# Kernel tuning notes

Hardware: AMD Instinct MI355X
Metric: run time of the kernel (lower is better)

The kernel has to match this reference:

```python
import math
import jax, jax.numpy as jnp
import numpy as np

HIDDEN = 1024
NUM_HEADS = 16
HEAD_DIM = HIDDEN // NUM_HEADS
B, S = 4, 2048


def setup_inputs() -> dict:
    key = jax.random.key(0)
    ks = jax.random.split(key, 10)
    sc_in = 1.0 / math.sqrt(HIDDEN)
    inp = {
        "query": jax.random.normal(ks[0], (B, S, HIDDEN), jnp.float32),
        "key": jax.random.normal(ks[1], (B, S, HIDDEN), jnp.float32),
        "value": jax.random.normal(ks[2], (B, S, HIDDEN), jnp.float32),
        "mask": jax.random.randint(ks[3], (B, S), 0, 2).astype(bool),
        # NOTE: ModuleList([Linear]*num_heads) shares ONE Linear across all heads.
        "Wq": jax.random.normal(ks[4], (HIDDEN, HEAD_DIM), jnp.float32) * sc_in,
        "bq": jnp.zeros((HEAD_DIM,), jnp.float32),
        "Wk": jax.random.normal(ks[5], (HIDDEN, HEAD_DIM), jnp.float32) * sc_in,
        "bk": jnp.zeros((HEAD_DIM,), jnp.float32),
        "Wv": jax.random.normal(ks[6], (HIDDEN, HEAD_DIM), jnp.float32) * sc_in,
        "bv": jnp.zeros((HEAD_DIM,), jnp.float32),
        "Wout": jax.random.normal(ks[7], (HIDDEN, HIDDEN), jnp.float32) * sc_in,
        "bout": jnp.zeros((HIDDEN,), jnp.float32),
        "seq_mask": 0,
    }
    return inp


def _layer_norm_scores(x, eps=1e-8):
    # torch.std is unbiased (ddof=1); is_train=False => no affine
    mean = jnp.mean(x, axis=-1, keepdims=True)
    sigma = jnp.std(x, axis=-1, keepdims=True, ddof=1)
    return (x - mean) / (sigma + eps)


def reference(query, key, value, mask, Wq, bq, Wk, bk, Wv, bv, Wout, bout, seq_mask):
    # All heads share identical weights -> compute one head, tile the concat.
    q = query @ Wq + bq          # [B,S,hd]
    k = key @ Wk + bk            # [B,S,hd]
    v = value @ Wv + bv          # [B,S,hd]
    scores = jnp.einsum("bqd,bkd->bqk", q, k) / math.sqrt(HIDDEN)  # [B,S,S]
    scores = _layer_norm_scores(scores)
    m = jnp.broadcast_to(mask[:, None, :], scores.shape)  # [B,S,S]
    if seq_mask:
        tri = jnp.triu(jnp.ones(scores.shape[-2:], bool), k=1)
        m = m | tri[None]
    # original fills with -1e-32 (effectively a no-op bug) -- reproduce exactly
    scores = scores + jnp.where(m, jnp.float32(-1e-32), jnp.float32(0.0))
    attn = jax.nn.softmax(scores, axis=-1)
    head = jnp.einsum("bqk,bkd->bqd", attn, v)   # [B,S,hd]
    attention = jnp.tile(head, (1, 1, NUM_HEADS))  # concat of identical heads
    return attention @ Wout + bout
```

## Files before the change

### kernel.cpp

```cpp
#include <hip/hip_runtime.h>
#include <math.h>

#define B_  4
#define S_  2048
#define H_  1024
#define D_  64
#define ROWS (B_*S_)
#define KSPLIT 16
#define LOG2E 1.4426950408889634f

typedef __attribute__((ext_vector_type(4))) float  floatx4;
typedef __attribute__((ext_vector_type(8))) short  short8;
typedef __attribute__((ext_vector_type(8))) __bf16 bf16x8;

#define WS_KSUM 0
#define WS_M    (WS_KSUM + B_*D_)
#define WS_A2   (WS_M + B_*D_*D_)
#define WS_C2   (WS_A2 + ROWS)
#define WS_SWP  (WS_C2 + ROWS)
#define WS_FEND (WS_SWP + KSPLIT*ROWS)
#define WB_QB  0
#define WB_KF  (WB_QB + ROWS*D_)
#define WB_VF  (WB_KF + ROWS*D_)
#define WB_WT  (WB_VF + ROWS*D_)
#define WB_WFF (WB_WT + 3*D_*H_)
#define WB_OP  (WB_WFF + H_*D_)
#define NZ2    (B_*D_ + B_*D_*D_)

__device__ __forceinline__ unsigned short f2bf(float f) {
    union { float f; unsigned u; } v; v.f = f;
    unsigned r = v.u + 0x7FFFu + ((v.u >> 16) & 1u);
    return (unsigned short)(r >> 16);
}
__device__ __forceinline__ short bfc(float f) {
    __bf16 h = (__bf16)f;
    short s; __builtin_memcpy(&s, &h, 2); return s;
}
__device__ __forceinline__ float bf2f(short s) {
    union { unsigned u; float f; } v;
    v.u = ((unsigned)(unsigned short)s) << 16; return v.f;
}
__device__ __forceinline__ bf16x8 ldb(const short* p) {
    union { short8 s; bf16x8 b; } u; u.s = *(const short8*)p; return u.b;
}
#define MFMA(a,b,c) __builtin_amdgcn_mfma_f32_16x16x32_bf16(a, b, c, 0, 0, 0)
__device__ __forceinline__ void lds_fence() {
    __builtin_amdgcn_wave_barrier();
    __builtin_amdgcn_s_waitcnt(0xc07f);
    __builtin_amdgcn_wave_barrier();
}

__global__ __launch_bounds__(256) void prep(
    const float* __restrict__ Wq, const float* __restrict__ Wk,
    const float* __restrict__ Wv, const float* __restrict__ Wout,
    float* __restrict__ wsf)
{
    __shared__ float tile[64][65];
    short* wsb = (short*)(wsf + WS_FEND);
    const int bx = blockIdx.x, t = threadIdx.x;
    if (bx < 96) {
        int idx = bx * 256 + t;
        int mat = idx >> 13, rem = idx & 8191;
        int kc = rem >> 8, nt = (rem >> 6) & 3, lane = rem & 63;
        int g = lane >> 4, l15 = lane & 15;
        const float* W = (mat == 0) ? Wq : (mat == 1) ? Wk : Wv;
        short8 fr;
        #pragma unroll
        for (int j = 0; j < 8; ++j)
            fr[j] = (short)f2bf(W[(size_t)(kc*32 + g*8 + j) * D_ + nt*16 + l15]);
        *(short8*)&wsb[WB_WT + (size_t)idx * 8] = fr;
    } else if (bx < 112) {
        int n0 = (bx - 96) * 64;
        int nn = t & 63, dg = t >> 6;
        for (int dd = 0; dd < 16; ++dd) {
            int d = dg * 16 + dd;
            float s = 0.0f;
            #pragma unroll
            for (int h = 0; h < 16; ++h)
                s += Wout[(size_t)(h * 64 + d) * H_ + n0 + nn];
            tile[d][nn] = s;
        }
        __syncthreads();
        #pragma unroll
        for (int u = 0; u < 2; ++u) {
            int s = 2*t + u;
            int ctl = s >> 7, h = (s >> 6) & 1, lane = s & 63;
            int g = lane >> 4, l2 = lane & 15;
            short8 fr;
            #pragma unroll
            for (int j = 0; j < 8; ++j)
                fr[j] = (short)f2bf(tile[h*32 + g*8 + j][ctl*16 + l2]);
            *(short8*)&wsb[WB_WFF + (size_t)((((n0 >> 4) + ctl)*2 + h)*64 + lane) * 8] = fr;
        }
    } else {
        int i = (bx - 112) * 256 + t;
        if (i < NZ2) wsf[WS_KSUM + i] = 0.0f;
    }
}

__global__ __launch_bounds__(256) void qkv_mfma(
    const float* __restrict__ query, const float* __restrict__ key,
    const float* __restrict__ value,
    const float* __restrict__ bq, const float* __restrict__ bk,
    const float* __restrict__ bvp, float* __restrict__ wsf)
{
    short* wsb = (short*)(wsf + WS_FEND);
    const int mat = blockIdx.y;
    const float* X    = (mat == 0) ? query : (mat == 1) ? key : value;
    const float* bias = (mat == 0) ? bq    : (mat == 1) ? bk  : bvp;
    const short* WT3 = wsb + WB_WT + (size_t)mat * (D_ * H_);

    const int t = threadIdx.x, w = t >> 6, lane = t & 63;
    const int l15 = lane & 15, g = lane >> 4;
    const int r0 = blockIdx.x * 32;
    const int mrow0 = (w >> 1) * 16;
    const int nt0 = (w & 1) * 2;

    __shared__ short xs[32][136];
    floatx4 acc[2] = {};

    for (int step = 0; step < 8; ++step) {
        __syncthreads();
        #pragma unroll
        for (int u = 0; u < 4; ++u) {
            int row = u * 8 + (t >> 5), col = (t & 31) * 4;
            float4 xv = *(const float4*)&X[(size_t)(r0 + row) * H_ + step * 128 + col];
            short4 pk;
            pk.x = bfc(xv.x); pk.y = bfc(xv.y); pk.z = bfc(xv.z); pk.w = bfc(xv.w);
            *(short4*)&xs[row][col] = pk;
        }
        __syncthreads();
        #pragma unroll
        for (int kk = 0; kk < 4; ++kk) {
            bf16x8 a = ldb(&xs[mrow0 + l15][kk * 32 + g * 8]);
            int kc = step * 4 + kk;
            #pragma unroll
            for (int n = 0; n < 2; ++n) {
                bf16x8 bf = ldb(&WT3[(size_t)((kc * 4) + nt0 + n) * 512 + lane * 8]);
                acc[n] = MFMA(a, bf, acc[n]);
            }
        }
    }

    if (mat == 0) {
        short* QB = wsb + WB_QB;
        #pragma unroll
        for (int n = 0; n < 2; ++n) {
            int col = (nt0 + n) * 16 + l15;
            float bb = bias[col];
            #pragma unroll
            for (int r = 0; r < 4; ++r)
                QB[(size_t)(r0 + mrow0 + 4*g + r) * D_ + col] = (short)f2bf(acc[n][r] + bb);
        }
    } else if (mat == 1) {
        short* KF = wsb + WB_KF;
        #pragma unroll
        for (int n = 0; n < 2; ++n) {
            int d = (nt0 + n) * 16 + l15;
            int kh = d >> 5, gk = (d >> 3) & 3, j = d & 7;
            float bb = bias[d];
            #pragma unroll
            for (int r = 0; r < 4; ++r) {
                int R = r0 + mrow0 + 4*g + r;
                KF[(size_t)(((R >> 4) * 2 + kh) * 64 + gk * 16 + (R & 15)) * 8 + j] =
                    (short)f2bf(acc[n][r] + bb);
            }
        }
    } else {
        short* VF = wsb + WB_VF;
        int R0 = r0 + mrow0 + 4*g;
        int kh = (R0 >> 5) & 1, gv = (R0 >> 3) & 3, j0 = R0 & 7, blk = R0 >> 6;
        #pragma unroll
        for (int n = 0; n < 2; ++n) {
            int d = (nt0 + n) * 16 + l15;
            int ntv = d >> 4;
            float bb = bias[d];
            short4 pk;
            pk.x = (short)f2bf(acc[n][0] + bb); pk.y = (short)f2bf(acc[n][1] + bb);
            pk.z = (short)f2bf(acc[n][2] + bb); pk.w = (short)f2bf(acc[n][3] + bb);
            *(short4*)&VF[(size_t)(((blk * 4 + ntv) * 2 + kh) * 64 + gv * 16 + (d & 15)) * 8 + j0] = pk;
        }
    }
}

__global__ __launch_bounds__(256) void kstats(float* __restrict__ wsf) {
    const short* KF = (short*)(wsf + WS_FEND) + WB_KF;
    const int b     = blockIdx.x >> 5;
    const int chunk = blockIdx.x & 31;
    const int keyblk0 = b * 128 + chunk * 4;

    __shared__ float kt[64][64];
    const int t = threadIdx.x;
    #pragma unroll
    for (int u = 0; u < 2; ++u) {
        int s = 2*t + u;
        int kb4 = s >> 7, kh = (s >> 6) & 1, lane2 = s & 63;
        int g2 = lane2 >> 4, l2 = lane2 & 15;
        short8 v = *(const short8*)&KF[(size_t)(((keyblk0 + kb4) * 2 + kh) * 64 + lane2) * 8];
        #pragma unroll
        for (int j = 0; j < 8; ++j)
            kt[kb4 * 16 + l2][kh * 32 + g2 * 8 + j] = bf2f(v[j]);
    }
    __syncthreads();

    const int td = t >> 4, te = t & 15;
    float acc[4][4] = {};
    for (int j = 0; j < 64; ++j) {
        float4 a  = *(const float4*)&kt[j][td*4];
        float4 bb = *(const float4*)&kt[j][te*4];
        float av[4] = {a.x, a.y, a.z, a.w};
        float bw[4] = {bb.x, bb.y, bb.z, bb.w};
        #pragma unroll
        for (int i = 0; i < 4; ++i)
            #pragma unroll
            for (int l = 0; l < 4; ++l)
                acc[i][l] += av[i] * bw[l];
    }
    float* M = wsf + WS_M + (size_t)b * D_ * D_;
    #pragma unroll
    for (int i = 0; i < 4; ++i)
        #pragma unroll
        for (int l = 0; l < 4; ++l)
            atomicAdd(&M[(td*4 + i) * D_ + te*4 + l], acc[i][l]);

    if (t < 64) {
        float s = 0.0f;
        for (int j = 0; j < 64; ++j) s += kt[j][t];
        atomicAdd(&wsf[WS_KSUM + b * D_ + t], s);
    }
}

__global__ __launch_bounds__(256) void rowstats(float* __restrict__ wsf) {
    const short* Qb = (short*)(wsf + WS_FEND) + WB_QB;
    const int t = threadIdx.x, w = t >> 6, lane = t & 63;
    const int q0 = blockIdx.x * 32 + w * 8;
    const int b  = q0 >> 11;
    const float* M = wsf + WS_M + (size_t)b * D_ * D_;

    float qv[8], y[8] = {};
    #pragma unroll
    for (int r = 0; r < 8; ++r) qv[r] = bf2f(Qb[(size_t)(q0 + r) * D_ + lane]);
    for (int d2 = 0; d2 < 64; ++d2) {
        float m = M[d2 * D_ + lane];
        #pragma unroll
        for (int r = 0; r < 8; ++r) y[r] += __shfl(qv[r], d2, 64) * m;
    }
    float kl = wsf[WS_KSUM + b * D_ + lane];
    float z[8], sv[8];
    #pragma unroll
    for (int r = 0; r < 8; ++r) { z[r] = y[r] * qv[r]; sv[r] = qv[r] * kl; }
    #pragma unroll
    for (int m = 1; m < 64; m <<= 1) {
        #pragma unroll
        for (int r = 0; r < 8; ++r) {
            z[r]  += __shfl_xor(z[r],  m, 64);
            sv[r] += __shfl_xor(sv[r], m, 64);
        }
    }
    #pragma unroll
    for (int r = 0; r < 8; ++r) {
        if (lane == r) {
            float sum   = sv[r] * (1.0f / 32.0f);
            float sumsq = z[r]  * (1.0f / 1024.0f);
            float mu  = sum * (1.0f / 2048.0f);
            float var = (sumsq - sum * sum * (1.0f / 2048.0f)) * (1.0f / 2047.0f);
            var = fmaxf(var, 0.0f);
            float inv = 1.0f / (sqrtf(var) + 1e-8f);
            wsf[WS_A2 + q0 + r] = inv * (LOG2E / 32.0f);
            wsf[WS_C2 + q0 + r] = -mu * inv * LOG2E;
        }
    }
}

__global__ __launch_bounds__(128, 3) void attention(float* __restrict__ wsf) {
    short* wsb = (short*)(wsf + WS_FEND);
    const short* Qb = wsb + WB_QB;
    const short* KF = wsb + WB_KF;
    const short* VF = wsb + WB_VF;
    __shared__ short P[2][32][72];

    const int t = threadIdx.x, w = t >> 6, lane = t & 63;
    const int l15 = lane & 15, g = lane >> 4;
    const int q0 = blockIdx.x * 64 + w * 32;
    const int b  = blockIdx.x >> 5;
    const int kb = blockIdx.y * (S_ / KSPLIT);

    bf16x8 bqf[2][2];
    float a2v[2], c2v[2];
    #pragma unroll
    for (int nt = 0; nt < 2; ++nt) {
        int q = q0 + nt*16 + l15;
        #pragma unroll
        for (int h = 0; h < 2; ++h)
            bqf[nt][h] = ldb(&Qb[(size_t)q * D_ + h*32 + g*8]);
        a2v[nt] = wsf[WS_A2 + q];
        c2v[nt] = wsf[WS_C2 + q];
    }

    floatx4 O[2][4] = {};
    float sacc[2] = {0.0f, 0.0f};
    short* Pw = &P[w][0][0];

    for (int kc = 0; kc < S_ / KSPLIT; kc += 64) {
        const int key0 = kb + kc;
        const int kblk16 = (b * S_ + key0) >> 4;
        const int kblk64 = (b * S_ + key0) >> 6;
        floatx4 Sc[4][2] = {};
        __builtin_amdgcn_s_setprio(1);
        #pragma unroll
        for (int kt = 0; kt < 4; ++kt) {
            bf16x8 ak0 = ldb(&KF[(size_t)(((kblk16 + kt) * 2 + 0) * 64 + lane) * 8]);
            bf16x8 ak1 = ldb(&KF[(size_t)(((kblk16 + kt) * 2 + 1) * 64 + lane) * 8]);
            #pragma unroll
            for (int nt = 0; nt < 2; ++nt) {
                Sc[kt][nt] = MFMA(ak0, bqf[nt][0], Sc[kt][nt]);
                Sc[kt][nt] = MFMA(ak1, bqf[nt][1], Sc[kt][nt]);
            }
        }
        __builtin_amdgcn_s_setprio(0);
        lds_fence();
        #pragma unroll
        for (int nt = 0; nt < 2; ++nt) {
            const float aa = a2v[nt], cc = c2v[nt];
            #pragma unroll
            for (int kt = 0; kt < 4; ++kt) {
                float w0 = __builtin_amdgcn_exp2f(fmaf(Sc[kt][nt][0], aa, cc));
                float w1 = __builtin_amdgcn_exp2f(fmaf(Sc[kt][nt][1], aa, cc));
                float w2 = __builtin_amdgcn_exp2f(fmaf(Sc[kt][nt][2], aa, cc));
                float w3 = __builtin_amdgcn_exp2f(fmaf(Sc[kt][nt][3], aa, cc));
                sacc[nt] += (w0 + w1) + (w2 + w3);
                short4 pk;
                pk.x = bfc(w0); pk.y = bfc(w1); pk.z = bfc(w2); pk.w = bfc(w3);
                *(short4*)&Pw[(nt*16 + l15) * 72 + kt*16 + 4*g] = pk;
            }
        }
        lds_fence();
        bf16x8 ap[2][2];
        #pragma unroll
        for (int mt = 0; mt < 2; ++mt)
            #pragma unroll
            for (int kh = 0; kh < 2; ++kh)
                ap[mt][kh] = ldb(&Pw[(mt*16 + l15) * 72 + kh*32 + g*8]);
        __builtin_amdgcn_s_setprio(1);
        #pragma unroll
        for (int nt = 0; nt < 4; ++nt) {
            #pragma unroll
            for (int kh = 0; kh < 2; ++kh) {
                bf16x8 bv = ldb(&VF[(size_t)(((kblk64 * 4 + nt) * 2 + kh) * 64 + lane) * 8]);
                #pragma unroll
                for (int mt = 0; mt < 2; ++mt)
                    O[mt][nt] = MFMA(ap[mt][kh], bv, O[mt][nt]);
            }
        }
        __builtin_amdgcn_s_setprio(0);
    }

    #pragma unroll
    for (int nt = 0; nt < 2; ++nt) {
        sacc[nt] += __shfl_xor(sacc[nt], 16, 64);
        sacc[nt] += __shfl_xor(sacc[nt], 32, 64);
    }
    if (lane < 16) {
        wsf[WS_SWP + blockIdx.y * ROWS + q0 + lane]      = sacc[0];
        wsf[WS_SWP + blockIdx.y * ROWS + q0 + 16 + lane] = sacc[1];
    }
    short* OP = wsb + WB_OP + ((size_t)blockIdx.y * ROWS + q0) * D_;
    #pragma unroll
    for (int mt = 0; mt < 2; ++mt)
        #pragma unroll
        for (int nt = 0; nt < 4; ++nt)
            #pragma unroll
            for (int r = 0; r < 4; ++r)
                OP[(size_t)(mt*16 + 4*g + r) * D_ + nt*16 + l15] =
                    (short)f2bf(O[mt][nt][r]);
}

__global__ __launch_bounds__(256) void outmm(
    const float* __restrict__ bout, const float* __restrict__ wsf,
    float* __restrict__ out)
{
    const short* wsb = (const short*)(wsf + WS_FEND);
    const short* OP  = wsb + WB_OP;
    const short* WFF = wsb + WB_WFF;
    __shared__ short hnF[2 * 64 * 8];

    const int t = threadIdx.x;
    const int row0 = blockIdx.x * 16;

    {
        const int r = t >> 4;
        const int c = (t & 15) * 4;
        const int row = row0 + r;
        float sw = 0.0f;
        #pragma unroll
        for (int p = 0; p < KSPLIT; ++p) sw += wsf[WS_SWP + p * ROWS + row];
        float inv = 1.0f / sw;
        float a0 = 0.f, a1 = 0.f, a2 = 0.f, a3 = 0.f;
        #pragma unroll
        for (int p = 0; p < KSPLIT; ++p) {
            short4 o = *(const short4*)&OP[((size_t)p * ROWS + row) * D_ + c];
            a0 += bf2f(o.x); a1 += bf2f(o.y); a2 += bf2f(o.z); a3 += bf2f(o.w);
        }
        short4 hn;
        hn.x = (short)f2bf(a0 * inv); hn.y = (short)f2bf(a1 * inv);
        hn.z = (short)f2bf(a2 * inv); hn.w = (short)f2bf(a3 * inv);
        int kh = c >> 5, gH = (c >> 3) & 3, j0 = c & 7;
        *(short4*)&hnF[(size_t)(kh * 64 + gH * 16 + r) * 8 + j0] = hn;
    }
    __syncthreads();

    const int w = t >> 6, lane = t & 63, l15 = lane & 15, g = lane >> 4;
    bf16x8 ah0 = ldb(&hnF[(size_t)(0 * 64 + lane) * 8]);
    bf16x8 ah1 = ldb(&hnF[(size_t)(1 * 64 + lane) * 8]);
    #pragma unroll
    for (int i = 0; i < 16; ++i) {
        int n16 = w * 16 + i;
        floatx4 acc = {};
        acc = MFMA(ah0, ldb(&WFF[(size_t)(n16 * 2 + 0) * 512 + lane * 8]), acc);
        acc = MFMA(ah1, ldb(&WFF[(size_t)(n16 * 2 + 1) * 512 + lane * 8]), acc);
        int col = n16 * 16 + l15;
        float bb = bout[col];
        #pragma unroll
        for (int r = 0; r < 4; ++r)
            out[(size_t)(row0 + 4*g + r) * H_ + col] = acc[r] + bb;
    }
}

extern "C" void kernel_launch(void* const* d_in, const int* in_sizes, int n_in,
                              void* d_out, int out_size, void* d_ws, size_t ws_size,
                              hipStream_t stream) {
    const float* query = (const float*)d_in[0];
    const float* key   = (const float*)d_in[1];
    const float* value = (const float*)d_in[2];
    const float* Wq   = (const float*)d_in[4];
    const float* bq   = (const float*)d_in[5];
    const float* Wk   = (const float*)d_in[6];
    const float* bk   = (const float*)d_in[7];
    const float* Wv   = (const float*)d_in[8];
    const float* bv   = (const float*)d_in[9];
    const float* Wout = (const float*)d_in[10];
    const float* bout = (const float*)d_in[11];

    float* ws  = (float*)d_ws;
    float* out = (float*)d_out;

    prep<<<177, 256, 0, stream>>>(Wq, Wk, Wv, Wout, ws);
    qkv_mfma<<<dim3(ROWS/32, 3), 256, 0, stream>>>(query, key, value, bq, bk, bv, ws);
    kstats<<<B_ * 32, 256, 0, stream>>>(ws);
    rowstats<<<ROWS/32, 256, 0, stream>>>(ws);
    attention<<<dim3(ROWS/64, KSPLIT), 128, 0, stream>>>(ws);
    outmm<<<ROWS/16, 256, 0, stream>>>(bout, ws, out);
}
```

Before: 204.0 us.

## Fuse split-K attention with output projection in one workgroup per query tile

Replaces the 16-way split-K attention kernel and the separate output-projection kernel with one kernel. Each 512-thread workgroup handles 16 query rows. Its 8 waves each cover 256 keys, and their partial O and row sums are reduced in LDS before the final Wout MFMA and store. This removes the global round trip of the bf16 partials and row sums, plus one launch. In exchange, each wave now reuses K/V across only 16 queries instead of 32, which raises K/V load traffic per MFMA, and the workgroup needs more LDS.

```diff
diff --git a/kernel.cpp b/kernel.cpp
--- a/kernel.cpp
+++ b/kernel.cpp
@@ -6,7 +6,6 @@
 #define H_  1024
 #define D_  64
 #define ROWS (B_*S_)
-#define KSPLIT 16
 #define LOG2E 1.4426950408889634f
 
 typedef __attribute__((ext_vector_type(4))) float  floatx4;
@@ -17,14 +16,12 @@
 #define WS_M    (WS_KSUM + B_*D_)
 #define WS_A2   (WS_M + B_*D_*D_)
 #define WS_C2   (WS_A2 + ROWS)
-#define WS_SWP  (WS_C2 + ROWS)
-#define WS_FEND (WS_SWP + KSPLIT*ROWS)
+#define WS_FEND (WS_C2 + ROWS)
 #define WB_QB  0
 #define WB_KF  (WB_QB + ROWS*D_)
 #define WB_VF  (WB_KF + ROWS*D_)
 #define WB_WT  (WB_VF + ROWS*D_)
 #define WB_WFF (WB_WT + 3*D_*H_)
-#define WB_OP  (WB_WFF + H_*D_)
 #define NZ2    (B_*D_ + B_*D_*D_)
 
 __device__ __forceinline__ unsigned short f2bf(float f) {
@@ -272,149 +269,109 @@
     }
 }
 
-__global__ __launch_bounds__(128, 3) void attention(float* __restrict__ wsf) {
+__global__ __launch_bounds__(512, 4) void attn_fused(
+    const float* __restrict__ bout, float* __restrict__ wsf,
+    float* __restrict__ out)
+{
     short* wsb = (short*)(wsf + WS_FEND);
-    const short* Qb = wsb + WB_QB;
-    const short* KF = wsb + WB_KF;
-    const short* VF = wsb + WB_VF;
-    __shared__ short P[2][32][72];
+    const short* Qb  = wsb + WB_QB;
+    const short* KF  = wsb + WB_KF;
+    const short* VF  = wsb + WB_VF;
+    const short* WFF = wsb + WB_WFF;
+
+    __shared__ short P[8][16][72];
+    __shared__ short OL[8][16][64];
+    __shared__ float sumwL[8][16];
+    __shared__ short hnF[2 * 64 * 8];
 
     const int t = threadIdx.x, w = t >> 6, lane = t & 63;
     const int l15 = lane & 15, g = lane >> 4;
-    const int q0 = blockIdx.x * 64 + w * 32;
-    const int b  = blockIdx.x >> 5;
-    const int kb = blockIdx.y * (S_ / KSPLIT);
-
-    bf16x8 bqf[2][2];
-    float a2v[2], c2v[2];
-    #pragma unroll
-    for (int nt = 0; nt < 2; ++nt) {
-        int q = q0 + nt*16 + l15;
-        #pragma unroll
-        for (int h = 0; h < 2; ++h)
-            bqf[nt][h] = ldb(&Qb[(size_t)q * D_ + h*32 + g*8]);
-        a2v[nt] = wsf[WS_A2 + q];
-        c2v[nt] = wsf[WS_C2 + q];
-    }
-
-    floatx4 O[2][4] = {};
-    float sacc[2] = {0.0f, 0.0f};
+    const int q0 = blockIdx.x * 16;
+    const int b  = blockIdx.x >> 7;
+
+    bf16x8 bqf0 = ldb(&Qb[(size_t)(q0 + l15) * D_ + 0*32 + g*8]);
+    bf16x8 bqf1 = ldb(&Qb[(size_t)(q0 + l15) * D_ + 1*32 + g*8]);
+    const float a2v = wsf[WS_A2 + q0 + l15];
+    const float c2v = wsf[WS_C2 + q0 + l15];
+
+    floatx4 O[4] = {};
+    float sacc = 0.0f;
     short* Pw = &P[w][0][0];
 
-    for (int kc = 0; kc < S_ / KSPLIT; kc += 64) {
-        const int key0 = kb + kc;
+    for (int kc = 0; kc < 256; kc += 64) {
+        const int key0 = w * 256 + kc;
         const int kblk16 = (b * S_ + key0) >> 4;
         const int kblk64 = (b * S_ + key0) >> 6;
-        floatx4 Sc[4][2] = {};
+        floatx4 Sc[4] = {};
         __builtin_amdgcn_s_setprio(1);
         #pragma unroll
         for (int kt = 0; kt < 4; ++kt) {
             bf16x8 ak0 = ldb(&KF[(size_t)(((kblk16 + kt) * 2 + 0) * 64 + lane) * 8]);
             bf16x8 ak1 = ldb(&KF[(size_t)(((kblk16 + kt) * 2 + 1) * 64 + lane) * 8]);
-            #pragma unroll
-            for (int nt = 0; nt < 2; ++nt) {
-                Sc[kt][nt] = MFMA(ak0, bqf[nt][0], Sc[kt][nt]);
-                Sc[kt][nt] = MFMA(ak1, bqf[nt][1], Sc[kt][nt]);
-            }
+            Sc[kt] = MFMA(ak0, bqf0, Sc[kt]);
+            Sc[kt] = MFMA(ak1, bqf1, Sc[kt]);
         }
         __builtin_amdgcn_s_setprio(0);
         lds_fence();
         #pragma unroll
-        for (int nt = 0; nt < 2; ++nt) {
-            const float aa = a2v[nt], cc = c2v[nt];
-            #pragma unroll
-            for (int kt = 0; kt < 4; ++kt) {
-                float w0 = __builtin_amdgcn_exp2f(fmaf(Sc[kt][nt][0], aa, cc));
-                float w1 = __builtin_amdgcn_exp2f(fmaf(Sc[kt][nt][1], aa, cc));
-                float w2 = __builtin_amdgcn_exp2f(fmaf(Sc[kt][nt][2], aa, cc));
-                float w3 = __builtin_amdgcn_exp2f(fmaf(Sc[kt][nt][3], aa, cc));
-                sacc[nt] += (w0 + w1) + (w2 + w3);
-                short4 pk;
-                pk.x = bfc(w0); pk.y = bfc(w1); pk.z = bfc(w2); pk.w = bfc(w3);
-                *(short4*)&Pw[(nt*16 + l15) * 72 + kt*16 + 4*g] = pk;
-            }
+        for (int kt = 0; kt < 4; ++kt) {
+            float w0 = __builtin_amdgcn_exp2f(fmaf(Sc[kt][0], a2v, c2v));
+            float w1 = __builtin_amdgcn_exp2f(fmaf(Sc[kt][1], a2v, c2v));
+            float w2 = __builtin_amdgcn_exp2f(fmaf(Sc[kt][2], a2v, c2v));
+            float w3 = __builtin_amdgcn_exp2f(fmaf(Sc[kt][3], a2v, c2v));
+            sacc += (w0 + w1) + (w2 + w3);
+            short4 pk;
+            pk.x = bfc(w0); pk.y = bfc(w1); pk.z = bfc(w2); pk.w = bfc(w3);
+            *(short4*)&Pw[l15 * 72 + kt*16 + 4*g] = pk;
         }
         lds_fence();
-        bf16x8 ap[2][2];
-        #pragma unroll
-        for (int mt = 0; mt < 2; ++mt)
-            #pragma unroll
-            for (int kh = 0; kh < 2; ++kh)
-                ap[mt][kh] = ldb(&Pw[(mt*16 + l15) * 72 + kh*32 + g*8]);
+        bf16x8 ap0 = ldb(&Pw[l15 * 72 + 0*32 + g*8]);
+        bf16x8 ap1 = ldb(&Pw[l15 * 72 + 1*32 + g*8]);
         __builtin_amdgcn_s_setprio(1);
         #pragma unroll
         for (int nt = 0; nt < 4; ++nt) {
-            #pragma unroll
-            for (int kh = 0; kh < 2; ++kh) {
-                bf16x8 bv = ldb(&VF[(size_t)(((kblk64 * 4 + nt) * 2 + kh) * 64 + lane) * 8]);
-                #pragma unroll
-                for (int mt = 0; mt < 2; ++mt)
-                    O[mt][nt] = MFMA(ap[mt][kh], bv, O[mt][nt]);
-            }
+            bf16x8 bv0 = ldb(&VF[(size_t)(((kblk64 * 4 + nt) * 2 + 0) * 64 + lane) * 8]);
+            bf16x8 bv1 = ldb(&VF[(size_t)(((kblk64 * 4 + nt) * 2 + 1) * 64 + lane) * 8]);
+            O[nt] = MFMA(ap0, bv0, O[nt]);
+            O[nt] = MFMA(ap1, bv1, O[nt]);
         }
         __builtin_amdgcn_s_setprio(0);
     }
 
-    #pragma unroll
-    for (int nt = 0; nt < 2; ++nt) {
-        sacc[nt] += __shfl_xor(sacc[nt], 16, 64);
-        sacc[nt] += __shfl_xor(sacc[nt], 32, 64);
-    }
-    if (lane < 16) {
-        wsf[WS_SWP + blockIdx.y * ROWS + q0 + lane]      = sacc[0];
-        wsf[WS_SWP + blockIdx.y * ROWS + q0 + 16 + lane] = sacc[1];
-    }
-    short* OP = wsb + WB_OP + ((size_t)blockIdx.y * ROWS + q0) * D_;
-    #pragma unroll
-    for (int mt = 0; mt < 2; ++mt)
-        #pragma unroll
-        for (int nt = 0; nt < 4; ++nt)
-            #pragma unroll
-            for (int r = 0; r < 4; ++r)
-                OP[(size_t)(mt*16 + 4*g + r) * D_ + nt*16 + l15] =
-                    (short)f2bf(O[mt][nt][r]);
-}
-
-__global__ __launch_bounds__(256) void outmm(
-    const float* __restrict__ bout, const float* __restrict__ wsf,
-    float* __restrict__ out)
-{
-    const short* wsb = (const short*)(wsf + WS_FEND);
-    const short* OP  = wsb + WB_OP;
-    const short* WFF = wsb + WB_WFF;
-    __shared__ short hnF[2 * 64 * 8];
-
-    const int t = threadIdx.x;
-    const int row0 = blockIdx.x * 16;
+    sacc += __shfl_xor(sacc, 16, 64);
+    sacc += __shfl_xor(sacc, 32, 64);
+    if (lane < 16) sumwL[w][lane] = sacc;
+    #pragma unroll
+    for (int nt = 0; nt < 4; ++nt)
+        #pragma unroll
+        for (int r = 0; r < 4; ++r)
+            OL[w][4*g + r][nt*16 + l15] = (short)f2bf(O[nt][r]);
+    __syncthreads();
 
     {
-        const int r = t >> 4;
-        const int c = (t & 15) * 4;
-        const int row = row0 + r;
-        float sw = 0.0f;
-        #pragma unroll
-        for (int p = 0; p < KSPLIT; ++p) sw += wsf[WS_SWP + p * ROWS + row];
+        const int row = t >> 5;
+        const int c = (t & 31) * 2;
+        float s0 = 0.f, s1 = 0.f, sw = 0.f;
+        #pragma unroll
+        for (int p = 0; p < 8; ++p) {
+            s0 += bf2f(OL[p][row][c]);
+            s1 += bf2f(OL[p][row][c + 1]);
+            sw += sumwL[p][row];
+        }
         float inv = 1.0f / sw;
-        float a0 = 0.f, a1 = 0.f, a2 = 0.f, a3 = 0.f;
-        #pragma unroll
-        for (int p = 0; p < KSPLIT; ++p) {
-            short4 o = *(const short4*)&OP[((size_t)p * ROWS + row) * D_ + c];
-            a0 += bf2f(o.x); a1 += bf2f(o.y); a2 += bf2f(o.z); a3 += bf2f(o.w);
-        }
-        short4 hn;
-        hn.x = (short)f2bf(a0 * inv); hn.y = (short)f2bf(a1 * inv);
-        hn.z = (short)f2bf(a2 * inv); hn.w = (short)f2bf(a3 * inv);
-        int kh = c >> 5, gH = (c >> 3) & 3, j0 = c & 7;
-        *(short4*)&hnF[(size_t)(kh * 64 + gH * 16 + r) * 8 + j0] = hn;
+        short2 hn;
+        hn.x = (short)f2bf(s0 * inv);
+        hn.y = (short)f2bf(s1 * inv);
+        int kh = c >> 5, g2 = (c >> 3) & 3, j = c & 7;
+        *(short2*)&hnF[(kh * 64 + g2 * 16 + row) * 8 + j] = hn;
     }
     __syncthreads();
 
-    const int w = t >> 6, lane = t & 63, l15 = lane & 15, g = lane >> 4;
-    bf16x8 ah0 = ldb(&hnF[(size_t)(0 * 64 + lane) * 8]);
-    bf16x8 ah1 = ldb(&hnF[(size_t)(1 * 64 + lane) * 8]);
-    #pragma unroll
-    for (int i = 0; i < 16; ++i) {
-        int n16 = w * 16 + i;
+    bf16x8 ah0 = ldb(&hnF[(0 * 64 + lane) * 8]);
+    bf16x8 ah1 = ldb(&hnF[(1 * 64 + lane) * 8]);
+    #pragma unroll
+    for (int i = 0; i < 8; ++i) {
+        int n16 = w * 8 + i;
         floatx4 acc = {};
         acc = MFMA(ah0, ldb(&WFF[(size_t)(n16 * 2 + 0) * 512 + lane * 8]), acc);
         acc = MFMA(ah1, ldb(&WFF[(size_t)(n16 * 2 + 1) * 512 + lane * 8]), acc);
@@ -422,7 +379,7 @@
         float bb = bout[col];
         #pragma unroll
         for (int r = 0; r < 4; ++r)
-            out[(size_t)(row0 + 4*g + r) * H_ + col] = acc[r] + bb;
+            out[(size_t)(q0 + 4*g + r) * H_ + col] = acc[r] + bb;
     }
 }
 
@@ -448,6 +405,5 @@
     qkv_mfma<<<dim3(ROWS/32, 3), 256, 0, stream>>>(query, key, value, bq, bk, bv, ws);
     kstats<<<B_ * 32, 256, 0, stream>>>(ws);
     rowstats<<<ROWS/32, 256, 0, stream>>>(ws);
-    attention<<<dim3(ROWS/64, KSPLIT), 128, 0, stream>>>(ws);
-    outmm<<<ROWS/16, 256, 0, stream>>>(bout, ws, out);
-}
+    attn_fused<<<ROWS/16, 512, 0, stream>>>(bout, ws, out);
+}
```

After: 204.9 us. Within noise of the previous version (+0.5%).
